# Kernel optimization log

Measured on AMD Instinct MI355X. Metric: run time of the kernel, lower is better.

The kernel has to match this reference:

```python
import jax, jax.numpy as jnp
import numpy as np

B, M, D, DP = 8192, 64, 128, 128

def setup_inputs() -> dict:
    key = jax.random.key(0)
    kx, kq, kk, kv, kr = jax.random.split(key, 5)
    scale = 1.0 / np.sqrt(D)  # keep softmax logits in a sane range
    return {
        "x": jax.random.normal(kx, (B, M, D), dtype=jnp.float32),
        "Wq": jax.random.normal(kq, (D, DP), dtype=jnp.float32) * scale,
        "Wk": jax.random.normal(kk, (D, DP), dtype=jnp.float32) * scale,
        "Wv": jax.random.normal(kv, (D, DP), dtype=jnp.float32) * scale,
        "Wr": jax.random.normal(kr, (D, DP), dtype=jnp.float32) * scale,
    }

def reference(x, Wq, Wk, Wv, Wr):
    # Shared per-field linear projections (Product layer): [B, M, d] @ [d, d'] -> [B, M, d']
    q = jnp.einsum('bmd,de->bme', x, Wq)
    k = jnp.einsum('bmd,de->bme', x, Wk)
    v = jnp.einsum('bmd,de->bme', x, Wv)
    r = jnp.einsum('bmd,de->bme', x, Wr)
    # Field-wise attention: scores [B, M, M], softmax over last axis (axis=2)
    scores = jnp.einsum('bme,bne->bmn', q, k)
    alphas = jax.nn.softmax(scores, axis=2)
    new_e = jnp.einsum('bmn,bne->bme', alphas, v)
    return jax.nn.relu(r + new_e)
```

## Files before the change

### kernel.cpp

```cpp
#include <hip/hip_runtime.h>

typedef _Float16 half8 __attribute__((ext_vector_type(8)));
typedef _Float16 half4 __attribute__((ext_vector_type(4)));
typedef float floatx4 __attribute__((ext_vector_type(4)));

#define NB 8
#define SX 136
#define SVT 72
#define SP 80

__global__ void wconv_kernel(const float* __restrict__ Wq, const float* __restrict__ Wk,
                             const float* __restrict__ Wv, const float* __restrict__ Wr,
                             _Float16* __restrict__ Wh) {
    int idx = blockIdx.x * 256 + threadIdx.x;
    int row = idx >> 9;
    int col = idx & 511;
    const float* s = (col < 128) ? Wq : (col < 256) ? Wk : (col < 384) ? Wv : Wr;
    Wh[idx] = (_Float16)s[row * 128 + (col & 127)];
}

__global__ __launch_bounds__(512, 2)
void autoint_kernel(const float* __restrict__ xg, const _Float16* __restrict__ Wh,
                    float* __restrict__ outg) {
    const int tid  = threadIdx.x;
    const int w    = tid >> 6;
    const int lane = tid & 63;
    const int nn   = lane & 15;
    const int q    = lane >> 4;
    const long b0  = (long)blockIdx.x * NB;

    __shared__ _Float16 lds[31744];
    _Float16* Xs = lds;
    _Float16* Vt = lds;
    _Float16* Qs = lds + 9216;
    _Float16* Ks = lds + 17920;
    _Float16* Ps = lds + 26624;

    half8 wf[4][4];
    #pragma unroll
    for (int c = 0; c < 4; ++c) {
        int ctg;
        if (w < 4) ctg = 4 * w + c;
        else       ctg = (c < 2) ? (16 + 2 * (w - 4) + c) : (24 + 2 * (w - 4) + (c - 2));
        int col = ctg * 16 + nn;
        #pragma unroll
        for (int ks = 0; ks < 4; ++ks) {
            half8 f;
            #pragma unroll
            for (int i = 0; i < 8; ++i)
                f[i] = Wh[(ks * 32 + q * 8 + i) * 512 + col];
            wf[c][ks] = f;
        }
    }

    float4 pf[8];
    if (w < 4) {
        const float4* Xg = (const float4*)(xg + b0 * 8192);
        #pragma unroll
        for (int t = 0; t < 8; ++t) pf[t] = Xg[t * 256 + tid];
        #pragma unroll
        for (int t = 0; t < 8; ++t) {
            int g = t * 256 + tid;
            int row = g >> 5, c4 = (g & 31) * 4;
            half4 h = { (_Float16)pf[t].x, (_Float16)pf[t].y,
                        (_Float16)pf[t].z, (_Float16)pf[t].w };
            *(half4*)(Xs + row * SX + c4) = h;
        }
    }
    __syncthreads();

    for (int it = 0; it < NB; ++it) {
        const long b = b0 + it;

        if (w < 4 && it + 1 < NB) {
            const float4* Xg = (const float4*)(xg + (b + 1) * 8192);
            #pragma unroll
            for (int t = 0; t < 8; ++t) pf[t] = Xg[t * 256 + tid];
        }

        floatx4 acc[4][4];
        {
            floatx4 z = {0.f, 0.f, 0.f, 0.f};
            #pragma unroll
            for (int rt = 0; rt < 4; ++rt)
                #pragma unroll
                for (int c = 0; c < 4; ++c) acc[rt][c] = z;
        }
        #pragma unroll
        for (int ks = 0; ks < 4; ++ks) {
            half8 a[4];
            #pragma unroll
            for (int rt = 0; rt < 4; ++rt)
                a[rt] = *(const half8*)(Xs + (rt * 16 + nn) * SX + ks * 32 + q * 8);
            #pragma unroll
            for (int rt = 0; rt < 4; ++rt)
                #pragma unroll
                for (int c = 0; c < 4; ++c)
                    acc[rt][c] = __builtin_amdgcn_mfma_f32_16x16x32_f16(
                        a[rt], wf[c][ks], acc[rt][c], 0, 0, 0);
        }
        __syncthreads();

        if (w < 2) {
            #pragma unroll
            for (int rt = 0; rt < 4; ++rt)
                #pragma unroll
                for (int c = 0; c < 4; ++c) {
                    int f = (4 * w + c) * 16 + nn;
                    #pragma unroll
                    for (int r = 0; r < 4; ++r)
                        Qs[(rt * 16 + q * 4 + r) * SX + f] = (_Float16)acc[rt][c][r];
                }
        } else if (w < 4) {
            #pragma unroll
            for (int rt = 0; rt < 4; ++rt)
                #pragma unroll
                for (int c = 0; c < 4; ++c) {
                    int f = (4 * w + c - 8) * 16 + nn;
                    #pragma unroll
                    for (int r = 0; r < 4; ++r)
                        Ks[(rt * 16 + q * 4 + r) * SX + f] = (_Float16)acc[rt][c][r];
                }
        } else {
            int j = w - 4;
            #pragma unroll
            for (int rt = 0; rt < 4; ++rt)
                #pragma unroll
                for (int c = 0; c < 2; ++c) {
                    int f = (2 * j + c) * 16 + nn;
                    half4 hv = { (_Float16)acc[rt][c][0], (_Float16)acc[rt][c][1],
                                 (_Float16)acc[rt][c][2], (_Float16)acc[rt][c][3] };
                    *(half4*)(Vt + f * SVT + rt * 16 + q * 4) = hv;
                }
        }
        __syncthreads();

        if (w < 4) {
            floatx4 sacc[4];
            {
                floatx4 z = {0.f, 0.f, 0.f, 0.f};
                #pragma unroll
                for (int c = 0; c < 4; ++c) sacc[c] = z;
            }
            #pragma unroll
            for (int ks = 0; ks < 4; ++ks) {
                half8 aq = *(const half8*)(Qs + (w * 16 + nn) * SX + ks * 32 + q * 8);
                #pragma unroll
                for (int c = 0; c < 4; ++c) {
                    half8 bk = *(const half8*)(Ks + (c * 16 + nn) * SX + ks * 32 + q * 8);
                    sacc[c] = __builtin_amdgcn_mfma_f32_16x16x32_f16(aq, bk, sacc[c], 0, 0, 0);
                }
            }
            #pragma unroll
            for (int r = 0; r < 4; ++r) {
                float mx = fmaxf(fmaxf(sacc[0][r], sacc[1][r]), fmaxf(sacc[2][r], sacc[3][r]));
                mx = fmaxf(mx, __shfl_xor(mx, 1));
                mx = fmaxf(mx, __shfl_xor(mx, 2));
                mx = fmaxf(mx, __shfl_xor(mx, 4));
                mx = fmaxf(mx, __shfl_xor(mx, 8));
                float e0 = __expf(sacc[0][r] - mx);
                float e1 = __expf(sacc[1][r] - mx);
                float e2 = __expf(sacc[2][r] - mx);
                float e3 = __expf(sacc[3][r] - mx);
                float s = e0 + e1 + e2 + e3;
                s += __shfl_xor(s, 1);
                s += __shfl_xor(s, 2);
                s += __shfl_xor(s, 4);
                s += __shfl_xor(s, 8);
                float inv = 1.0f / s;
                int row = w * 16 + q * 4 + r;
                Ps[row * SP + 0 * 16 + nn] = (_Float16)(e0 * inv);
                Ps[row * SP + 1 * 16 + nn] = (_Float16)(e1 * inv);
                Ps[row * SP + 2 * 16 + nn] = (_Float16)(e2 * inv);
                Ps[row * SP + 3 * 16 + nn] = (_Float16)(e3 * inv);
            }
        }
        __syncthreads();

        if (w >= 4) {
            int j = w - 4;
            floatx4 pv[4][2];
            {
                floatx4 z = {0.f, 0.f, 0.f, 0.f};
                #pragma unroll
                for (int rt = 0; rt < 4; ++rt) { pv[rt][0] = z; pv[rt][1] = z; }
            }
            #pragma unroll
            for (int ks = 0; ks < 2; ++ks) {
                half8 ap[4];
                #pragma unroll
                for (int rt = 0; rt < 4; ++rt)
                    ap[rt] = *(const half8*)(Ps + (rt * 16 + nn) * SP + ks * 32 + q * 8);
                #pragma unroll
                for (int cl = 0; cl < 2; ++cl) {
                    half8 bv = *(const half8*)(Vt + ((2 * j + cl) * 16 + nn) * SVT + ks * 32 + q * 8);
                    #pragma unroll
                    for (int rt = 0; rt < 4; ++rt)
                        pv[rt][cl] = __builtin_amdgcn_mfma_f32_16x16x32_f16(ap[rt], bv, pv[rt][cl], 0, 0, 0);
                }
            }
            float* ob = outg + b * 8192;
            #pragma unroll
            for (int rt = 0; rt < 4; ++rt)
                #pragma unroll
                for (int cl = 0; cl < 2; ++cl) {
                    int colb = (2 * j + cl) * 16 + nn;
                    #pragma unroll
                    for (int r = 0; r < 4; ++r) {
                        int row = rt * 16 + q * 4 + r;
                        float v = acc[rt][2 + cl][r] + pv[rt][cl][r];
                        ob[row * 128 + colb] = fmaxf(v, 0.0f);
                    }
                }
        }
        __syncthreads();

        if (w < 4 && it + 1 < NB) {
            #pragma unroll
            for (int t = 0; t < 8; ++t) {
                int g = t * 256 + tid;
                int row = g >> 5, c4 = (g & 31) * 4;
                half4 h = { (_Float16)pf[t].x, (_Float16)pf[t].y,
                            (_Float16)pf[t].z, (_Float16)pf[t].w };
                *(half4*)(Xs + row * SX + c4) = h;
            }
        }
        __syncthreads();
    }
}

extern "C" void kernel_launch(void* const* d_in, const int* in_sizes, int n_in,
                              void* d_out, int out_size, void* d_ws, size_t ws_size,
                              hipStream_t stream) {
    const float* x  = (const float*)d_in[0];
    const float* Wq = (const float*)d_in[1];
    const float* Wk = (const float*)d_in[2];
    const float* Wv = (const float*)d_in[3];
    const float* Wr = (const float*)d_in[4];
    _Float16* Wh = (_Float16*)d_ws;
    float* out = (float*)d_out;

    wconv_kernel<<<256, 256, 0, stream>>>(Wq, Wk, Wv, Wr, Wh);
    autoint_kernel<<<1024, 512, 0, stream>>>(x, Wh, out);
}
```

Before: 478.2 us.

## Double-buffer X, balance projections across all waves, keep softmax probabilities in registers

Each of the 8 waves now computes a 16-column slice of all four projections (Q, K, V, R), so projection work is balanced across the block. X is double-buffered in LDS so the next batch can be written before the barrier, which cuts the per-iteration barriers from five to two. Scores are computed transposed so the softmax reduces within a lane and across 16-lane groups. The fp16 probabilities are then rearranged with lane shuffles straight into MFMA A-operands instead of going through LDS. The costs are larger LDS use (R is now stored in fp16 and V is kept in its own buffer), which may limit occupancy, plus extra shuffle and rounding work.

Measured after the change: 468.7 us. 2.0% less time.

```diff
diff --git a/kernel.cpp b/kernel.cpp
--- a/kernel.cpp
+++ b/kernel.cpp
@@ -2,12 +2,12 @@
 
 typedef _Float16 half8 __attribute__((ext_vector_type(8)));
 typedef _Float16 half4 __attribute__((ext_vector_type(4)));
+typedef __fp16 fp16x2 __attribute__((ext_vector_type(2)));
 typedef float floatx4 __attribute__((ext_vector_type(4)));
 
 #define NB 8
 #define SX 136
 #define SVT 72
-#define SP 80
 
 __global__ void wconv_kernel(const float* __restrict__ Wq, const float* __restrict__ Wk,
                              const float* __restrict__ Wv, const float* __restrict__ Wr,
@@ -27,55 +27,57 @@
     const int lane = tid & 63;
     const int nn   = lane & 15;
     const int q    = lane >> 4;
+    const int qp   = q & 1, qh = q >> 1;
     const long b0  = (long)blockIdx.x * NB;
 
-    __shared__ _Float16 lds[31744];
-    _Float16* Xs = lds;
-    _Float16* Vt = lds;
-    _Float16* Qs = lds + 9216;
-    _Float16* Ks = lds + 17920;
-    _Float16* Ps = lds + 26624;
+    __shared__ _Float16 lds[52736];
+    _Float16* Xs0 = lds;
+    _Float16* Xs1 = lds + 8704;
+    _Float16* Qs  = lds + 17408;
+    _Float16* Ks  = lds + 26112;
+    _Float16* Rs  = lds + 34816;
+    _Float16* Vt  = lds + 43520;
 
     half8 wf[4][4];
     #pragma unroll
-    for (int c = 0; c < 4; ++c) {
-        int ctg;
-        if (w < 4) ctg = 4 * w + c;
-        else       ctg = (c < 2) ? (16 + 2 * (w - 4) + c) : (24 + 2 * (w - 4) + (c - 2));
-        int col = ctg * 16 + nn;
+    for (int g = 0; g < 4; ++g) {
+        const int col = g * 128 + w * 16 + nn;
         #pragma unroll
         for (int ks = 0; ks < 4; ++ks) {
             half8 f;
             #pragma unroll
             for (int i = 0; i < 8; ++i)
                 f[i] = Wh[(ks * 32 + q * 8 + i) * 512 + col];
-            wf[c][ks] = f;
+            wf[g][ks] = f;
         }
     }
 
-    float4 pf[8];
-    if (w < 4) {
+    float4 pf[4];
+    {
         const float4* Xg = (const float4*)(xg + b0 * 8192);
         #pragma unroll
-        for (int t = 0; t < 8; ++t) pf[t] = Xg[t * 256 + tid];
-        #pragma unroll
-        for (int t = 0; t < 8; ++t) {
-            int g = t * 256 + tid;
+        for (int t = 0; t < 4; ++t) pf[t] = Xg[t * 512 + tid];
+        #pragma unroll
+        for (int t = 0; t < 4; ++t) {
+            int g = t * 512 + tid;
             int row = g >> 5, c4 = (g & 31) * 4;
             half4 h = { (_Float16)pf[t].x, (_Float16)pf[t].y,
                         (_Float16)pf[t].z, (_Float16)pf[t].w };
-            *(half4*)(Xs + row * SX + c4) = h;
+            *(half4*)(Xs0 + row * SX + c4) = h;
         }
     }
     __syncthreads();
 
+    #pragma unroll 2
     for (int it = 0; it < NB; ++it) {
         const long b = b0 + it;
-
-        if (w < 4 && it + 1 < NB) {
+        const _Float16* Xc = (it & 1) ? Xs1 : Xs0;
+        _Float16*       Xn = (it & 1) ? Xs0 : Xs1;
+
+        if (it + 1 < NB) {
             const float4* Xg = (const float4*)(xg + (b + 1) * 8192);
             #pragma unroll
-            for (int t = 0; t < 8; ++t) pf[t] = Xg[t * 256 + tid];
+            for (int t = 0; t < 4; ++t) pf[t] = Xg[t * 512 + tid];
         }
 
         floatx4 acc[4][4];
@@ -84,147 +86,152 @@
             #pragma unroll
             for (int rt = 0; rt < 4; ++rt)
                 #pragma unroll
-                for (int c = 0; c < 4; ++c) acc[rt][c] = z;
+                for (int g = 0; g < 4; ++g) acc[rt][g] = z;
         }
         #pragma unroll
         for (int ks = 0; ks < 4; ++ks) {
             half8 a[4];
             #pragma unroll
             for (int rt = 0; rt < 4; ++rt)
-                a[rt] = *(const half8*)(Xs + (rt * 16 + nn) * SX + ks * 32 + q * 8);
+                a[rt] = *(const half8*)(Xc + (rt * 16 + nn) * SX + ks * 32 + q * 8);
             #pragma unroll
             for (int rt = 0; rt < 4; ++rt)
                 #pragma unroll
-                for (int c = 0; c < 4; ++c)
-                    acc[rt][c] = __builtin_amdgcn_mfma_f32_16x16x32_f16(
-                        a[rt], wf[c][ks], acc[rt][c], 0, 0, 0);
-        }
-        __syncthreads();
-
-        if (w < 2) {
-            #pragma unroll
-            for (int rt = 0; rt < 4; ++rt)
-                #pragma unroll
-                for (int c = 0; c < 4; ++c) {
-                    int f = (4 * w + c) * 16 + nn;
-                    #pragma unroll
-                    for (int r = 0; r < 4; ++r)
-                        Qs[(rt * 16 + q * 4 + r) * SX + f] = (_Float16)acc[rt][c][r];
-                }
-        } else if (w < 4) {
-            #pragma unroll
-            for (int rt = 0; rt < 4; ++rt)
-                #pragma unroll
-                for (int c = 0; c < 4; ++c) {
-                    int f = (4 * w + c - 8) * 16 + nn;
-                    #pragma unroll
-                    for (int r = 0; r < 4; ++r)
-                        Ks[(rt * 16 + q * 4 + r) * SX + f] = (_Float16)acc[rt][c][r];
-                }
-        } else {
-            int j = w - 4;
-            #pragma unroll
-            for (int rt = 0; rt < 4; ++rt)
-                #pragma unroll
-                for (int c = 0; c < 2; ++c) {
-                    int f = (2 * j + c) * 16 + nn;
-                    half4 hv = { (_Float16)acc[rt][c][0], (_Float16)acc[rt][c][1],
-                                 (_Float16)acc[rt][c][2], (_Float16)acc[rt][c][3] };
-                    *(half4*)(Vt + f * SVT + rt * 16 + q * 4) = hv;
-                }
-        }
-        __syncthreads();
-
-        if (w < 4) {
-            floatx4 sacc[4];
-            {
-                floatx4 z = {0.f, 0.f, 0.f, 0.f};
-                #pragma unroll
-                for (int c = 0; c < 4; ++c) sacc[c] = z;
-            }
-            #pragma unroll
-            for (int ks = 0; ks < 4; ++ks) {
-                half8 aq = *(const half8*)(Qs + (w * 16 + nn) * SX + ks * 32 + q * 8);
-                #pragma unroll
-                for (int c = 0; c < 4; ++c) {
-                    half8 bk = *(const half8*)(Ks + (c * 16 + nn) * SX + ks * 32 + q * 8);
-                    sacc[c] = __builtin_amdgcn_mfma_f32_16x16x32_f16(aq, bk, sacc[c], 0, 0, 0);
-                }
-            }
-            #pragma unroll
-            for (int r = 0; r < 4; ++r) {
-                float mx = fmaxf(fmaxf(sacc[0][r], sacc[1][r]), fmaxf(sacc[2][r], sacc[3][r]));
-                mx = fmaxf(mx, __shfl_xor(mx, 1));
-                mx = fmaxf(mx, __shfl_xor(mx, 2));
-                mx = fmaxf(mx, __shfl_xor(mx, 4));
-                mx = fmaxf(mx, __shfl_xor(mx, 8));
-                float e0 = __expf(sacc[0][r] - mx);
-                float e1 = __expf(sacc[1][r] - mx);
-                float e2 = __expf(sacc[2][r] - mx);
-                float e3 = __expf(sacc[3][r] - mx);
-                float s = e0 + e1 + e2 + e3;
-                s += __shfl_xor(s, 1);
-                s += __shfl_xor(s, 2);
-                s += __shfl_xor(s, 4);
-                s += __shfl_xor(s, 8);
-                float inv = 1.0f / s;
-                int row = w * 16 + q * 4 + r;
-                Ps[row * SP + 0 * 16 + nn] = (_Float16)(e0 * inv);
-                Ps[row * SP + 1 * 16 + nn] = (_Float16)(e1 * inv);
-                Ps[row * SP + 2 * 16 + nn] = (_Float16)(e2 * inv);
-                Ps[row * SP + 3 * 16 + nn] = (_Float16)(e3 * inv);
-            }
-        }
-        __syncthreads();
-
-        if (w >= 4) {
-            int j = w - 4;
-            floatx4 pv[4][2];
-            {
-                floatx4 z = {0.f, 0.f, 0.f, 0.f};
-                #pragma unroll
-                for (int rt = 0; rt < 4; ++rt) { pv[rt][0] = z; pv[rt][1] = z; }
-            }
-            #pragma unroll
-            for (int ks = 0; ks < 2; ++ks) {
-                half8 ap[4];
-                #pragma unroll
-                for (int rt = 0; rt < 4; ++rt)
-                    ap[rt] = *(const half8*)(Ps + (rt * 16 + nn) * SP + ks * 32 + q * 8);
-                #pragma unroll
-                for (int cl = 0; cl < 2; ++cl) {
-                    half8 bv = *(const half8*)(Vt + ((2 * j + cl) * 16 + nn) * SVT + ks * 32 + q * 8);
-                    #pragma unroll
-                    for (int rt = 0; rt < 4; ++rt)
-                        pv[rt][cl] = __builtin_amdgcn_mfma_f32_16x16x32_f16(ap[rt], bv, pv[rt][cl], 0, 0, 0);
-                }
-            }
-            float* ob = outg + b * 8192;
-            #pragma unroll
-            for (int rt = 0; rt < 4; ++rt)
-                #pragma unroll
-                for (int cl = 0; cl < 2; ++cl) {
-                    int colb = (2 * j + cl) * 16 + nn;
-                    #pragma unroll
-                    for (int r = 0; r < 4; ++r) {
-                        int row = rt * 16 + q * 4 + r;
-                        float v = acc[rt][2 + cl][r] + pv[rt][cl][r];
-                        ob[row * 128 + colb] = fmaxf(v, 0.0f);
-                    }
-                }
-        }
-        __syncthreads();
-
-        if (w < 4 && it + 1 < NB) {
-            #pragma unroll
-            for (int t = 0; t < 8; ++t) {
-                int g = t * 256 + tid;
+                for (int g = 0; g < 4; ++g)
+                    acc[rt][g] = __builtin_amdgcn_mfma_f32_16x16x32_f16(
+                        a[rt], wf[g][ks], acc[rt][g], 0, 0, 0);
+        }
+
+        const int fc = w * 16 + nn;
+        #pragma unroll
+        for (int rt = 0; rt < 4; ++rt) {
+            const int r0 = rt * 16 + q * 4;
+            #pragma unroll
+            for (int r = 0; r < 4; ++r) Qs[(r0 + r) * SX + fc] = (_Float16)acc[rt][0][r];
+            #pragma unroll
+            for (int r = 0; r < 4; ++r) Ks[(r0 + r) * SX + fc] = (_Float16)acc[rt][1][r];
+            half4 hv = { (_Float16)acc[rt][2][0], (_Float16)acc[rt][2][1],
+                         (_Float16)acc[rt][2][2], (_Float16)acc[rt][2][3] };
+            *(half4*)(Vt + fc * SVT + r0) = hv;
+            #pragma unroll
+            for (int r = 0; r < 4; ++r) Rs[(r0 + r) * SX + fc] = (_Float16)acc[rt][3][r];
+        }
+
+        if (it + 1 < NB) {
+            #pragma unroll
+            for (int t = 0; t < 4; ++t) {
+                int g = t * 512 + tid;
                 int row = g >> 5, c4 = (g & 31) * 4;
                 half4 h = { (_Float16)pf[t].x, (_Float16)pf[t].y,
                             (_Float16)pf[t].z, (_Float16)pf[t].w };
-                *(half4*)(Xs + row * SX + c4) = h;
-            }
-        }
+                *(half4*)(Xn + row * SX + c4) = h;
+            }
+        }
+
+        __syncthreads();
+
+        const int mt = w & 3;
+        const int eb = (w >> 2) * 4;
+
+        floatx4 sacc[4];
+        {
+            floatx4 z = {0.f, 0.f, 0.f, 0.f};
+            #pragma unroll
+            for (int nt = 0; nt < 4; ++nt) sacc[nt] = z;
+        }
+        #pragma unroll
+        for (int ks = 0; ks < 4; ++ks) {
+            half8 bq = *(const half8*)(Qs + (mt * 16 + nn) * SX + ks * 32 + q * 8);
+            #pragma unroll
+            for (int nt = 0; nt < 4; ++nt) {
+                half8 ak = *(const half8*)(Ks + (nt * 16 + nn) * SX + ks * 32 + q * 8);
+                sacc[nt] = __builtin_amdgcn_mfma_f32_16x16x32_f16(ak, bq, sacc[nt], 0, 0, 0);
+            }
+        }
+
+        float mx = sacc[0][0];
+        #pragma unroll
+        for (int nt = 0; nt < 4; ++nt)
+            #pragma unroll
+            for (int r = 0; r < 4; ++r) mx = fmaxf(mx, sacc[nt][r]);
+        mx = fmaxf(mx, __shfl_xor(mx, 16));
+        mx = fmaxf(mx, __shfl_xor(mx, 32));
+        float ex[4][4];
+        float sum = 0.f;
+        #pragma unroll
+        for (int nt = 0; nt < 4; ++nt)
+            #pragma unroll
+            for (int r = 0; r < 4; ++r) {
+                ex[nt][r] = __expf(sacc[nt][r] - mx);
+                sum += ex[nt][r];
+            }
+        sum += __shfl_xor(sum, 16);
+        sum += __shfl_xor(sum, 32);
+        const float inv = 1.0f / sum;
+
+        unsigned pku[4][2];
+        #pragma unroll
+        for (int nt = 0; nt < 4; ++nt)
+            #pragma unroll
+            for (int h = 0; h < 2; ++h) {
+                union { fp16x2 h2; unsigned u; } cv;
+                cv.h2 = __builtin_amdgcn_cvt_pkrtz(ex[nt][2 * h] * inv, ex[nt][2 * h + 1] * inv);
+                pku[nt][h] = cv.u;
+            }
+
+        unsigned af2[2][4];
+        #pragma unroll
+        for (int c = 0; c < 8; ++c) {
+            const int ks2 = (c >> 1) & 1;
+            const int h   = c & 1;
+            const int lo  = c >> 2;
+            unsigned gv = (qp ^ lo) ? pku[2 * ks2 + 1][h] : pku[2 * ks2][h];
+            int srcl = ((qp << 1) + (qh ^ lo)) * 16 + nn;
+            af2[ks2][h + 2 * lo] = (unsigned)__shfl((int)gv, srcl);
+        }
+        #pragma unroll
+        for (int ks2 = 0; ks2 < 2; ++ks2) {
+            unsigned a0 = af2[ks2][0], a1 = af2[ks2][1], a2 = af2[ks2][2], a3 = af2[ks2][3];
+            af2[ks2][0] = qh ? a2 : a0;
+            af2[ks2][1] = qh ? a3 : a1;
+            af2[ks2][2] = qh ? a0 : a2;
+            af2[ks2][3] = qh ? a1 : a3;
+        }
+        half8 af[2];
+        #pragma unroll
+        for (int ks2 = 0; ks2 < 2; ++ks2) {
+            union { unsigned u[4]; half8 h; } uu;
+            uu.u[0] = af2[ks2][0]; uu.u[1] = af2[ks2][1];
+            uu.u[2] = af2[ks2][2]; uu.u[3] = af2[ks2][3];
+            af[ks2] = uu.h;
+        }
+
+        floatx4 pv[4];
+        {
+            floatx4 z = {0.f, 0.f, 0.f, 0.f};
+            #pragma unroll
+            for (int cc = 0; cc < 4; ++cc) pv[cc] = z;
+        }
+        #pragma unroll
+        for (int ks2 = 0; ks2 < 2; ++ks2)
+            #pragma unroll
+            for (int cc = 0; cc < 4; ++cc) {
+                half8 bv = *(const half8*)(Vt + ((eb + cc) * 16 + nn) * SVT + ks2 * 32 + q * 8);
+                pv[cc] = __builtin_amdgcn_mfma_f32_16x16x32_f16(af[ks2], bv, pv[cc], 0, 0, 0);
+            }
+
+        float* ob = outg + b * 8192;
+        #pragma unroll
+        for (int cc = 0; cc < 4; ++cc) {
+            const int col = (eb + cc) * 16 + nn;
+            #pragma unroll
+            for (int r = 0; r < 4; ++r) {
+                const int row = mt * 16 + q * 4 + r;
+                float rv = (float)Rs[row * SX + col];
+                ob[row * 128 + col] = fmaxf(rv + pv[cc][r], 0.0f);
+            }
+        }
+
         __syncthreads();
     }
 }
```
